# Kernel optimization log

Hardware: AMD Instinct MI355X
Metric: run time of the kernel (lower is better)

The kernel has to match this reference:

```python
import jax, jax.numpy as jnp
import numpy as np

N_NODES = 50000
IN_C, HID, N_CLS = 128, 128, 16
N_EDGES = 800000


def gcn_conv(x, W, b, src, dst, deg_inv_sqrt, n_nodes):
    # PyG GCNConv: h = x @ W; out[dst] += norm * h[src]; out += b
    h = x @ W                                   # [N, out_c]
    norm = deg_inv_sqrt[src] * deg_inv_sqrt[dst]  # [E]
    msgs = h[src] * norm[:, None]               # gather + scale, [E, out_c]
    out = jax.ops.segment_sum(msgs, dst, num_segments=n_nodes)
    return out + b


def setup_inputs() -> dict:
    key = jax.random.key(0)
    k1, k2, k3, k4, k5 = jax.random.split(key, 5)
    x = jax.random.normal(k1, (N_NODES, IN_C), dtype=jnp.float32)
    edge_index = jax.random.randint(k2, (2, N_EDGES), 0, N_NODES, dtype=jnp.int64)
    # glorot-ish params (torch.manual_seed(1234) in source only affects init values)
    def lin(k, fan_in, fan_out):
        s = 1.0 / np.sqrt(fan_in)
        kw, kb = jax.random.split(k)
        W = jax.random.uniform(kw, (fan_in, fan_out), minval=-s, maxval=s, dtype=jnp.float32)
        b = jax.random.uniform(kb, (fan_out,), minval=-s, maxval=s, dtype=jnp.float32)
        return W, b
    W1, b1 = lin(k3, IN_C, HID)
    W2, b2 = lin(k4, HID, HID)
    Wh, bh = lin(k5, HID, N_CLS)
    return {"x": x, "edge_index": edge_index, "W1": W1, "b1": b1,
            "W2": W2, "b2": b2, "Wh": Wh, "bh": bh}


def reference(x, edge_index, W1, b1, W2, b2, Wh, bh):
    n = x.shape[0]
    # add self-loops (PyG GCNConv default add_self_loops=True)
    loops = jnp.arange(n, dtype=edge_index.dtype)
    src = jnp.concatenate([edge_index[0], loops])
    dst = jnp.concatenate([edge_index[1], loops])
    # symmetric normalization D^{-1/2} (A+I) D^{-1/2}; degree over dst with unit weights
    deg = jax.ops.segment_sum(jnp.ones(src.shape[0], dtype=x.dtype), dst, num_segments=n)
    dis = jnp.where(deg > 0, jax.lax.rsqrt(deg), 0.0)
    h = gcn_conv(x, W1, b1, src, dst, dis, n)
    h = jax.nn.relu(h)
    h = gcn_conv(h, W2, b2, src, dst, dis, n)
    h = jax.nn.relu(h)
    return h @ Wh + bh
```

## Files before the change

### kernel.cpp

```cpp
#include <hip/hip_runtime.h>

#define CH 128
#define NCLS 16
#define CHK 16
#define NCHUNK 8
#define ECAP 131072

typedef __attribute__((ext_vector_type(8))) short bf16x8;
typedef __attribute__((ext_vector_type(4))) float f32x4;

__device__ inline ushort f2bf(float f) {
    unsigned u = __float_as_uint(f);
    unsigned r = u + 0x7fffu + ((u >> 16) & 1u);
    return (ushort)(r >> 16);
}
__device__ inline float bf2f(ushort b) {
    return __uint_as_float(((unsigned)b) << 16);
}

__global__ __launch_bounds__(256) void prep_kernel(
    const float* __restrict__ W1, const float* __restrict__ W2,
    ushort* __restrict__ w1hi, ushort* __restrict__ w1lo,
    ushort* __restrict__ w2hi, ushort* __restrict__ w2lo,
    int* __restrict__ cnt, int* __restrict__ pcnt, int* __restrict__ galloc,
    float* __restrict__ bufA, int n, int nbz) {
    int b = blockIdx.x, tid = threadIdx.x;
    if (b < 128) {
        const float* W = (b < 64) ? W1 : W2;
        ushort* Whi = (b < 64) ? w1hi : w2hi;
        ushort* Wlo = (b < 64) ? w1lo : w2lo;
        int t = ((b & 63) << 8) + tid;
        int k = t >> 7, nn = t & 127;
        float v = W[t];
        ushort h = f2bf(v);
        Whi[nn * CH + k] = h;
        Wlo[nn * CH + k] = f2bf(v - bf2f(h));
    } else if (b < 128 + nbz) {
        int i = (b - 128) * 256 + tid;
        if (i < n) cnt[i] = 0;
    } else {
        if (tid < NCHUNK * CHK) {
            int c = tid >> 4, ch = tid & 15;
            bufA[((size_t)c * (n + 1) + n) * CHK + ch] = 0.0f;
        }
        if (tid < 8) pcnt[tid] = 0;
        if (tid == 8) *galloc = 0;
    }
}

__global__ __launch_bounds__(256) void bucketcount_kernel(
    const int* __restrict__ src, const int* __restrict__ dst,
    unsigned* __restrict__ ebuf, int* __restrict__ pcnt,
    int* __restrict__ cnt, int E, float p8n) {
    __shared__ int lpos[8];
    __shared__ int lbase[8];
    int tid = threadIdx.x;
    if (tid < 8) lpos[tid] = 0;
    __syncthreads();
    int i0 = (blockIdx.x * 256 + tid) * 4;
    int part[4]; int off[4]; unsigned pk[4]; int c = 0;
    if (i0 + 3 < E) {
        int4 s4 = *(const int4*)&src[i0];
        int4 d4 = *(const int4*)&dst[i0];
        int ss[4] = {s4.x, s4.y, s4.z, s4.w};
        int dd[4] = {d4.x, d4.y, d4.z, d4.w};
        c = 4;
#pragma unroll
        for (int k = 0; k < 4; k++) {
            part[k] = min(7, (int)((float)dd[k] * p8n));
            pk[k] = ((unsigned)dd[k] << 16) | (unsigned)ss[k];
            off[k] = atomicAdd(&lpos[part[k]], 1);
            atomicAdd(&cnt[dd[k]], 1);
        }
    } else {
        for (int k = 0; k < 4 && i0 + k < E; k++) {
            int s = src[i0 + k], d = dst[i0 + k];
            part[c] = min(7, (int)((float)d * p8n));
            pk[c] = ((unsigned)d << 16) | (unsigned)s;
            off[c] = atomicAdd(&lpos[part[c]], 1);
            atomicAdd(&cnt[d], 1);
            c++;
        }
    }
    __syncthreads();
    if (tid < 8) lbase[tid] = atomicAdd(&pcnt[tid], lpos[tid]);
    __syncthreads();
    for (int k = 0; k < c; k++) {
        int idx = lbase[part[k]] + off[k];
        if (idx < ECAP) ebuf[(size_t)part[k] * ECAP + idx] = pk[k];
    }
}

__global__ __launch_bounds__(256) void place_kernel(
    const int* __restrict__ cnt, int* __restrict__ rsp,
    int* __restrict__ cursor, int* __restrict__ galloc,
    ushort* __restrict__ esrc, int n) {
    __shared__ int lds[256];
    __shared__ int gbase;
    int t = threadIdx.x;
    int i = blockIdx.x * 256 + t;
    int c = (i < n) ? cnt[i] : 0;
    int sz = (i < n) ? ((c + 8) & ~7) : 0;
    lds[t] = sz;
    __syncthreads();
    for (int off = 1; off < 256; off <<= 1) {
        int x = (t >= off) ? lds[t - off] : 0;
        __syncthreads();
        lds[t] += x;
        __syncthreads();
    }
    int incl = lds[t];
    if (t == 255) gbase = atomicAdd(galloc, incl);
    __syncthreads();
    int base = gbase + incl - sz;
    if (i < n) {
        rsp[i] = base;
        cursor[i] = base + 1;
        esrc[base] = (ushort)i;
        for (int p = base + 1 + c; p < base + sz; p++) esrc[p] = (ushort)n;
    }
}

template <bool RELU_IN>
__device__ __forceinline__ void gemm_body(
    int bx, int by, const float* __restrict__ A,
    const ushort* __restrict__ Bthi, const ushort* __restrict__ Btlo,
    const int* __restrict__ cntp, float* __restrict__ C, int n_rows) {
    const int tid = threadIdx.x;
    const int bm0 = bx * 128;
    const int wv = tid >> 6;
    const int lane = tid & 63;
    const int col = lane & 15;
    const int quad = lane >> 4;
    const int rbase = bm0 + wv * 32 + col;
    const int ntBase = by * 4;

    f32x4 acc[2][4];
#pragma unroll
    for (int m = 0; m < 2; m++)
#pragma unroll
        for (int t = 0; t < 4; t++) acc[m][t] = (f32x4){0.f, 0.f, 0.f, 0.f};

#pragma unroll
    for (int k0 = 0; k0 < 4; k0++) {
        const int kb = k0 * 32 + quad * 8;
        bf16x8 ah[2], al[2];
#pragma unroll
        for (int m = 0; m < 2; m++) {
            int arow = rbase + m * 16;
            bool av = (arow < n_rows);
            const float* __restrict__ Ap = A + (size_t)arow * CH + kb;
            float4 f0 = av ? *(const float4*)Ap       : make_float4(0.f, 0.f, 0.f, 0.f);
            float4 f1 = av ? *(const float4*)(Ap + 4) : make_float4(0.f, 0.f, 0.f, 0.f);
            if (RELU_IN) {
                f0.x = fmaxf(f0.x, 0.f); f0.y = fmaxf(f0.y, 0.f);
                f0.z = fmaxf(f0.z, 0.f); f0.w = fmaxf(f0.w, 0.f);
                f1.x = fmaxf(f1.x, 0.f); f1.y = fmaxf(f1.y, 0.f);
                f1.z = fmaxf(f1.z, 0.f); f1.w = fmaxf(f1.w, 0.f);
            }
            float fa[8] = {f0.x, f0.y, f0.z, f0.w, f1.x, f1.y, f1.z, f1.w};
#pragma unroll
            for (int j = 0; j < 8; j++) {
                ushort h = f2bf(fa[j]);
                ah[m][j] = (short)h;
                al[m][j] = (short)f2bf(fa[j] - bf2f(h));
            }
        }
#pragma unroll
        for (int t = 0; t < 4; t++) {
            const int boff = ((ntBase + t) * 16 + col) * CH + kb;
            bf16x8 bh = *(const bf16x8*)&Bthi[boff];
            bf16x8 bl = *(const bf16x8*)&Btlo[boff];
#pragma unroll
            for (int m = 0; m < 2; m++) {
                acc[m][t] = __builtin_amdgcn_mfma_f32_16x16x32_bf16(ah[m], bh, acc[m][t], 0, 0, 0);
                acc[m][t] = __builtin_amdgcn_mfma_f32_16x16x32_bf16(ah[m], bl, acc[m][t], 0, 0, 0);
                acc[m][t] = __builtin_amdgcn_mfma_f32_16x16x32_bf16(al[m], bh, acc[m][t], 0, 0, 0);
            }
        }
    }

#pragma unroll
    for (int m = 0; m < 2; m++) {
#pragma unroll
        for (int reg = 0; reg < 4; reg++) {
            int gr = bm0 + wv * 32 + m * 16 + quad * 4 + reg;
            if (gr < n_rows) {
                float d = rsqrtf((float)cntp[gr] + 1.0f);
#pragma unroll
                for (int t = 0; t < 4; t++) {
                    int nt = ntBase + t;
                    __builtin_nontemporal_store(
                        acc[m][t][reg] * d,
                        &C[((size_t)nt * (n_rows + 1) + gr) * CHK + col]);
                }
            }
        }
    }
}

template <bool RELU_IN>
__global__ __launch_bounds__(256, 4) void gemmfill_kernel(
    const float* __restrict__ A, const ushort* __restrict__ Bthi,
    const ushort* __restrict__ Btlo, const int* __restrict__ cntp,
    float* __restrict__ C, int n_rows, int nbx, int gemmBlocks,
    const unsigned* __restrict__ ebuf, const int* __restrict__ pcnt,
    int* __restrict__ cursor, ushort* __restrict__ esrc) {
    int b = blockIdx.x;
    if (b < gemmBlocks) {
        gemm_body<RELU_IN>(b % nbx, b / nbx, A, Bthi, Btlo, cntp, C, n_rows);
    } else {
        int fb = b - gemmBlocks;
        int part = fb & 7;
        int m = min(pcnt[part], ECAP);
        const unsigned* bk = ebuf + (size_t)part * ECAP;
        for (int e = (fb >> 3) * 256 + (int)threadIdx.x; e < m; e += 256 * 256) {
            unsigned pe = bk[e];
            int p = atomicAdd(&cursor[pe >> 16], 1);
            esrc[p] = (ushort)(pe & 0xffffu);
        }
    }
}

__global__ __launch_bounds__(256) void gather_kernel(
    const int* __restrict__ rsp, const int* __restrict__ cnt,
    const ushort* __restrict__ esrc, const float* __restrict__ hC,
    const float* __restrict__ bias, float* __restrict__ out, int n) {
    int c = blockIdx.x & 7;
    int wv = threadIdx.x >> 6;
    int lane = threadIdx.x & 63;
    int g = lane >> 2;
    int q = lane & 3;
    int i = (blockIdx.x >> 3) * 64 + wv * 16 + g;
    bool valid = (i < n);
    int iw = valid ? i : 0;
    const float4* __restrict__ h4 = (const float4*)(hC + (size_t)c * (n + 1) * CHK);

    float warm = 0.f;
    {
        int nblk = (n + 63) >> 6;
        size_t p = (size_t)(blockIdx.x >> 3) * 256 + threadIdx.x;
        size_t sliceF4 = ((size_t)(n + 1) * CHK) >> 2;
        for (; p < sliceF4; p += (size_t)nblk * 256) {
            float4 v = h4[p];
            warm += v.x + v.y + v.z + v.w;
        }
    }

    int beg = valid ? rsp[iw] : 0;
    int cv  = valid ? cnt[iw] : -8;
    int pc  = (cv + 8) & ~7;
    float4 acc = make_float4(0.f, 0.f, 0.f, 0.f);
    for (int j = beg; j < beg + pc; j += 8) {
        ushort4 e0 = *(const ushort4*)&esrc[j];
        ushort4 e1 = *(const ushort4*)&esrc[j + 4];
        float4 v0 = h4[(size_t)e0.x * 4 + q];
        float4 v1 = h4[(size_t)e0.y * 4 + q];
        float4 v2 = h4[(size_t)e0.z * 4 + q];
        float4 v3 = h4[(size_t)e0.w * 4 + q];
        float4 v4 = h4[(size_t)e1.x * 4 + q];
        float4 v5 = h4[(size_t)e1.y * 4 + q];
        float4 v6 = h4[(size_t)e1.z * 4 + q];
        float4 v7 = h4[(size_t)e1.w * 4 + q];
        acc.x += v0.x; acc.y += v0.y; acc.z += v0.z; acc.w += v0.w;
        acc.x += v1.x; acc.y += v1.y; acc.z += v1.z; acc.w += v1.w;
        acc.x += v2.x; acc.y += v2.y; acc.z += v2.z; acc.w += v2.w;
        acc.x += v3.x; acc.y += v3.y; acc.z += v3.z; acc.w += v3.w;
        acc.x += v4.x; acc.y += v4.y; acc.z += v4.z; acc.w += v4.w;
        acc.x += v5.x; acc.y += v5.y; acc.z += v5.z; acc.w += v5.w;
        acc.x += v6.x; acc.y += v6.y; acc.z += v6.z; acc.w += v6.w;
        acc.x += v7.x; acc.y += v7.y; acc.z += v7.z; acc.w += v7.w;
    }
    __asm__ volatile("" : : "v"(warm));
    if (valid) {
        float di = rsqrtf((float)cv + 1.0f);
        float4 bv = ((const float4*)bias)[c * 4 + q];
        f32x4 o;
        o[0] = bv.x + di * acc.x;
        o[1] = bv.y + di * acc.y;
        o[2] = bv.z + di * acc.z;
        o[3] = bv.w + di * acc.w;
        __builtin_nontemporal_store(o, (f32x4*)&((float4*)out)[(size_t)iw * 32 + c * 4 + q]);
    }
}

__global__ __launch_bounds__(256) void head_kernel(
    const float* __restrict__ A, const float* __restrict__ Wh,
    const float* __restrict__ bh, float* __restrict__ out, int n) {
    __shared__ float Ws[CH * NCLS];
    __shared__ float As[16][129];
    const int tid = threadIdx.x;
    const int n0 = blockIdx.x * 16;
#pragma unroll
    for (int i = 0; i < 8; i++) {
        int l = tid + i * 256;
        Ws[l] = Wh[l];
    }
#pragma unroll
    for (int i = 0; i < 8; i++) {
        int l = tid + i * 256;
        int r = l >> 7, c = l & 127;
        int gr = n0 + r;
        As[r][c] = (gr < n) ? fmaxf(A[(size_t)gr * CH + c], 0.0f) : 0.0f;
    }
    __syncthreads();
    int r = tid >> 4, c = tid & 15;
    float acc = bh[c];
#pragma unroll
    for (int k = 0; k < CH; k++) acc = fmaf(As[r][k], Ws[k * NCLS + c], acc);
    int gr = n0 + r;
    if (gr < n) out[(size_t)gr * NCLS + c] = acc;
}

extern "C" void kernel_launch(void* const* d_in, const int* in_sizes, int n_in,
                              void* d_out, int out_size, void* d_ws, size_t ws_size,
                              hipStream_t stream) {
    const float* x  = (const float*)d_in[0];
    const int*   ei = (const int*)d_in[1];
    const float* W1 = (const float*)d_in[2];
    const float* b1 = (const float*)d_in[3];
    const float* W2 = (const float*)d_in[4];
    const float* b2 = (const float*)d_in[5];
    const float* Wh = (const float*)d_in[6];
    const float* bh = (const float*)d_in[7];
    float* out = (float*)d_out;

    const int n = in_sizes[0] / CH;
    const int E = in_sizes[1] / 2;
    const int* src = ei;
    const int* dst = ei + E;

    ushort* w1hi = (ushort*)d_ws;
    ushort* w1lo = w1hi + CH * CH;
    ushort* w2hi = w1lo + CH * CH;
    ushort* w2lo = w2hi + CH * CH;
    float* bufA = (float*)(w2lo + CH * CH);
    float* bufB = bufA + (size_t)(n + 1) * CH;
    int* cnt    = (int*)(bufB + (size_t)n * CH);
    int* rsp    = cnt + n;
    int* cursor = rsp + n;
    int* pcnt   = cursor + n;
    int* galloc = pcnt + 8;
    ushort* esrc = (ushort*)(pcnt + 16);
    unsigned* ebuf = (unsigned*)bufB;

    const int B = 256;
    const int nbz = (n + B - 1) / B;
    const int nbx = (n + 127) / 128;
    const int gemmBlocks = nbx * 2;
    const float p8n = 8.0f / (float)n;

    prep_kernel<<<128 + nbz + 1, B, 0, stream>>>(W1, W2, w1hi, w1lo, w2hi, w2lo,
                                                 cnt, pcnt, galloc, bufA, n, nbz);
    bucketcount_kernel<<<(E + 1023) / 1024, B, 0, stream>>>(src, dst, ebuf, pcnt,
                                                            cnt, E, p8n);
    place_kernel<<<nbz, B, 0, stream>>>(cnt, rsp, cursor, galloc, esrc, n);

    const int gatherGrid = NCHUNK * ((n + 63) / 64);

    gemmfill_kernel<false><<<gemmBlocks + 2048, B, 0, stream>>>(
        x, w1hi, w1lo, cnt, bufA, n, nbx, gemmBlocks, ebuf, pcnt, cursor, esrc);
    gather_kernel<<<gatherGrid, B, 0, stream>>>(rsp, cnt, esrc, bufA, b1, bufB, n);
    gemmfill_kernel<true><<<gemmBlocks, B, 0, stream>>>(
        bufB, w2hi, w2lo, cnt, bufA, n, nbx, gemmBlocks, ebuf, pcnt, cursor, esrc);
    gather_kernel<<<gatherGrid, B, 0, stream>>>(rsp, cnt, esrc, bufA, b2, bufB, n);
    head_kernel<<<(n + 15) / 16, B, 0, stream>>>(bufB, Wh, bh, out, n);
}
```

Measured before the change: 296.4 us.

## Store intermediate GEMM output as fp16 and gather in 32-channel chunks

The GEMM epilogue now writes the degree-scaled hidden features as packed fp16 instead of fp32. The chunked layout changes from 8 chunks of 16 channels to 4 chunks of 32, so each gather lane loads 8 halves per neighbor and accumulates in fp32. This halves the bytes moved by the gather and the cache warm-up pass and halves the gather grid. In exchange it adds fp16 rounding error on the intermediate activations, and the output values could exceed fp16 range.

```diff
diff --git a/kernel.cpp b/kernel.cpp
--- a/kernel.cpp
+++ b/kernel.cpp
@@ -2,12 +2,13 @@
 
 #define CH 128
 #define NCLS 16
-#define CHK 16
-#define NCHUNK 8
+#define CHK 32
+#define NCHUNK 4
 #define ECAP 131072
 
 typedef __attribute__((ext_vector_type(8))) short bf16x8;
 typedef __attribute__((ext_vector_type(4))) float f32x4;
+typedef __attribute__((ext_vector_type(8))) _Float16 f16x8;
 
 __device__ inline ushort f2bf(float f) {
     unsigned u = __float_as_uint(f);
@@ -16,6 +17,12 @@
 }
 __device__ inline float bf2f(ushort b) {
     return __uint_as_float(((unsigned)b) << 16);
+}
+__device__ inline ushort f2h(float f) {
+    _Float16 h = (_Float16)f;
+    ushort u;
+    __builtin_memcpy(&u, &h, 2);
+    return u;
 }
 
 __global__ __launch_bounds__(256) void prep_kernel(
@@ -23,7 +30,7 @@
     ushort* __restrict__ w1hi, ushort* __restrict__ w1lo,
     ushort* __restrict__ w2hi, ushort* __restrict__ w2lo,
     int* __restrict__ cnt, int* __restrict__ pcnt, int* __restrict__ galloc,
-    float* __restrict__ bufA, int n, int nbz) {
+    ushort* __restrict__ hC, int n, int nbz) {
     int b = blockIdx.x, tid = threadIdx.x;
     if (b < 128) {
         const float* W = (b < 64) ? W1 : W2;
@@ -40,8 +47,8 @@
         if (i < n) cnt[i] = 0;
     } else {
         if (tid < NCHUNK * CHK) {
-            int c = tid >> 4, ch = tid & 15;
-            bufA[((size_t)c * (n + 1) + n) * CHK + ch] = 0.0f;
+            int c = tid >> 5, ch = tid & 31;
+            hC[((size_t)c * (n + 1) + n) * CHK + ch] = 0;
         }
         if (tid < 8) pcnt[tid] = 0;
         if (tid == 8) *galloc = 0;
@@ -125,7 +132,7 @@
 __device__ __forceinline__ void gemm_body(
     int bx, int by, const float* __restrict__ A,
     const ushort* __restrict__ Bthi, const ushort* __restrict__ Btlo,
-    const int* __restrict__ cntp, float* __restrict__ C, int n_rows) {
+    const int* __restrict__ cntp, ushort* __restrict__ C16, int n_rows) {
     const int tid = threadIdx.x;
     const int bm0 = bx * 128;
     const int wv = tid >> 6;
@@ -188,11 +195,15 @@
             if (gr < n_rows) {
                 float d = rsqrtf((float)cntp[gr] + 1.0f);
 #pragma unroll
-                for (int t = 0; t < 4; t++) {
-                    int nt = ntBase + t;
-                    __builtin_nontemporal_store(
-                        acc[m][t][reg] * d,
-                        &C[((size_t)nt * (n_rows + 1) + gr) * CHK + col]);
+                for (int tp = 0; tp < 4; tp += 2) {
+                    int nt0 = ntBase + tp;
+                    int chunk = nt0 >> 1;
+                    unsigned h0 = f2h(acc[m][tp][reg] * d);
+                    unsigned h1 = f2h(acc[m][tp + 1][reg] * d);
+                    unsigned pk = h0 | (h1 << 16);
+                    __builtin_nontemporal_store(pk,
+                        (unsigned*)&C16[((size_t)chunk * (n_rows + 1) + gr) * CHK
+                                        + 2 * col]);
                 }
             }
         }
@@ -203,12 +214,12 @@
 __global__ __launch_bounds__(256, 4) void gemmfill_kernel(
     const float* __restrict__ A, const ushort* __restrict__ Bthi,
     const ushort* __restrict__ Btlo, const int* __restrict__ cntp,
-    float* __restrict__ C, int n_rows, int nbx, int gemmBlocks,
+    ushort* __restrict__ C16, int n_rows, int nbx, int gemmBlocks,
     const unsigned* __restrict__ ebuf, const int* __restrict__ pcnt,
     int* __restrict__ cursor, ushort* __restrict__ esrc) {
     int b = blockIdx.x;
     if (b < gemmBlocks) {
-        gemm_body<RELU_IN>(b % nbx, b / nbx, A, Bthi, Btlo, cntp, C, n_rows);
+        gemm_body<RELU_IN>(b % nbx, b / nbx, A, Bthi, Btlo, cntp, C16, n_rows);
     } else {
         int fb = b - gemmBlocks;
         int part = fb & 7;
@@ -224,25 +235,27 @@
 
 __global__ __launch_bounds__(256) void gather_kernel(
     const int* __restrict__ rsp, const int* __restrict__ cnt,
-    const ushort* __restrict__ esrc, const float* __restrict__ hC,
+    const ushort* __restrict__ esrc, const ushort* __restrict__ hC16,
     const float* __restrict__ bias, float* __restrict__ out, int n) {
-    int c = blockIdx.x & 7;
+    int c = blockIdx.x & 3;
+    int bic = blockIdx.x >> 2;
     int wv = threadIdx.x >> 6;
     int lane = threadIdx.x & 63;
     int g = lane >> 2;
     int q = lane & 3;
-    int i = (blockIdx.x >> 3) * 64 + wv * 16 + g;
+    int i = bic * 64 + wv * 16 + g;
     bool valid = (i < n);
     int iw = valid ? i : 0;
-    const float4* __restrict__ h4 = (const float4*)(hC + (size_t)c * (n + 1) * CHK);
+    const f16x8* __restrict__ h8 = (const f16x8*)(hC16 + (size_t)c * (n + 1) * CHK);
 
     float warm = 0.f;
     {
-        int nblk = (n + 63) >> 6;
-        size_t p = (size_t)(blockIdx.x >> 3) * 256 + threadIdx.x;
-        size_t sliceF4 = ((size_t)(n + 1) * CHK) >> 2;
-        for (; p < sliceF4; p += (size_t)nblk * 256) {
-            float4 v = h4[p];
+        int nbr = (n + 63) >> 6;
+        const float4* __restrict__ w4 = (const float4*)h8;
+        size_t p = (size_t)bic * 256 + threadIdx.x;
+        size_t sliceF4 = ((size_t)(n + 1) * CHK) >> 3;
+        for (; p < sliceF4; p += (size_t)nbr * 256) {
+            float4 v = w4[p];
             warm += v.x + v.y + v.z + v.w;
         }
     }
@@ -250,37 +263,45 @@
     int beg = valid ? rsp[iw] : 0;
     int cv  = valid ? cnt[iw] : -8;
     int pc  = (cv + 8) & ~7;
-    float4 acc = make_float4(0.f, 0.f, 0.f, 0.f);
+    float accA[4] = {0.f, 0.f, 0.f, 0.f};
+    float accB[4] = {0.f, 0.f, 0.f, 0.f};
     for (int j = beg; j < beg + pc; j += 8) {
         ushort4 e0 = *(const ushort4*)&esrc[j];
         ushort4 e1 = *(const ushort4*)&esrc[j + 4];
-        float4 v0 = h4[(size_t)e0.x * 4 + q];
-        float4 v1 = h4[(size_t)e0.y * 4 + q];
-        float4 v2 = h4[(size_t)e0.z * 4 + q];
-        float4 v3 = h4[(size_t)e0.w * 4 + q];
-        float4 v4 = h4[(size_t)e1.x * 4 + q];
-        float4 v5 = h4[(size_t)e1.y * 4 + q];
-        float4 v6 = h4[(size_t)e1.z * 4 + q];
-        float4 v7 = h4[(size_t)e1.w * 4 + q];
-        acc.x += v0.x; acc.y += v0.y; acc.z += v0.z; acc.w += v0.w;
-        acc.x += v1.x; acc.y += v1.y; acc.z += v1.z; acc.w += v1.w;
-        acc.x += v2.x; acc.y += v2.y; acc.z += v2.z; acc.w += v2.w;
-        acc.x += v3.x; acc.y += v3.y; acc.z += v3.z; acc.w += v3.w;
-        acc.x += v4.x; acc.y += v4.y; acc.z += v4.z; acc.w += v4.w;
-        acc.x += v5.x; acc.y += v5.y; acc.z += v5.z; acc.w += v5.w;
-        acc.x += v6.x; acc.y += v6.y; acc.z += v6.z; acc.w += v6.w;
-        acc.x += v7.x; acc.y += v7.y; acc.z += v7.z; acc.w += v7.w;
+        f16x8 v0 = h8[(size_t)e0.x * 4 + q];
+        f16x8 v1 = h8[(size_t)e0.y * 4 + q];
+        f16x8 v2 = h8[(size_t)e0.z * 4 + q];
+        f16x8 v3 = h8[(size_t)e0.w * 4 + q];
+        f16x8 v4 = h8[(size_t)e1.x * 4 + q];
+        f16x8 v5 = h8[(size_t)e1.y * 4 + q];
+        f16x8 v6 = h8[(size_t)e1.z * 4 + q];
+        f16x8 v7 = h8[(size_t)e1.w * 4 + q];
+#pragma unroll
+        for (int s = 0; s < 4; s++) {
+            accA[s] += (float)v0[2 * s]; accB[s] += (float)v0[2 * s + 1];
+            accA[s] += (float)v1[2 * s]; accB[s] += (float)v1[2 * s + 1];
+            accA[s] += (float)v2[2 * s]; accB[s] += (float)v2[2 * s + 1];
+            accA[s] += (float)v3[2 * s]; accB[s] += (float)v3[2 * s + 1];
+            accA[s] += (float)v4[2 * s]; accB[s] += (float)v4[2 * s + 1];
+            accA[s] += (float)v5[2 * s]; accB[s] += (float)v5[2 * s + 1];
+            accA[s] += (float)v6[2 * s]; accB[s] += (float)v6[2 * s + 1];
+            accA[s] += (float)v7[2 * s]; accB[s] += (float)v7[2 * s + 1];
+        }
     }
     __asm__ volatile("" : : "v"(warm));
     if (valid) {
         float di = rsqrtf((float)cv + 1.0f);
-        float4 bv = ((const float4*)bias)[c * 4 + q];
-        f32x4 o;
-        o[0] = bv.x + di * acc.x;
-        o[1] = bv.y + di * acc.y;
-        o[2] = bv.z + di * acc.z;
-        o[3] = bv.w + di * acc.w;
-        __builtin_nontemporal_store(o, (f32x4*)&((float4*)out)[(size_t)iw * 32 + c * 4 + q]);
+        const float4* bias4 = (const float4*)bias;
+        float4 bvA = bias4[8 * c + q];
+        float4 bvB = bias4[8 * c + 4 + q];
+        f32x4 oA, oB;
+        oA[0] = bvA.x + di * accA[0]; oA[1] = bvA.y + di * accA[1];
+        oA[2] = bvA.z + di * accA[2]; oA[3] = bvA.w + di * accA[3];
+        oB[0] = bvB.x + di * accB[0]; oB[1] = bvB.y + di * accB[1];
+        oB[2] = bvB.z + di * accB[2]; oB[3] = bvB.w + di * accB[3];
+        float4* out4 = (float4*)out;
+        __builtin_nontemporal_store(oA, (f32x4*)&out4[(size_t)iw * 32 + 8 * c + q]);
+        __builtin_nontemporal_store(oB, (f32x4*)&out4[(size_t)iw * 32 + 8 * c + 4 + q]);
     }
 }
 
@@ -334,8 +355,8 @@
     ushort* w1lo = w1hi + CH * CH;
     ushort* w2hi = w1lo + CH * CH;
     ushort* w2lo = w2hi + CH * CH;
-    float* bufA = (float*)(w2lo + CH * CH);
-    float* bufB = bufA + (size_t)(n + 1) * CH;
+    ushort* hA  = w2lo + CH * CH;
+    float* bufB = (float*)(hA + (size_t)(n + 1) * CH);
     int* cnt    = (int*)(bufB + (size_t)n * CH);
     int* rsp    = cnt + n;
     int* cursor = rsp + n;
@@ -348,21 +369,21 @@
     const int nbz = (n + B - 1) / B;
     const int nbx = (n + 127) / 128;
     const int gemmBlocks = nbx * 2;
+    const int nbr = (n + 63) / 64;
+    const int gatherGrid = NCHUNK * nbr;
     const float p8n = 8.0f / (float)n;
 
     prep_kernel<<<128 + nbz + 1, B, 0, stream>>>(W1, W2, w1hi, w1lo, w2hi, w2lo,
-                                                 cnt, pcnt, galloc, bufA, n, nbz);
+                                                 cnt, pcnt, galloc, hA, n, nbz);
     bucketcount_kernel<<<(E + 1023) / 1024, B, 0, stream>>>(src, dst, ebuf, pcnt,
                                                             cnt, E, p8n);
     place_kernel<<<nbz, B, 0, stream>>>(cnt, rsp, cursor, galloc, esrc, n);
 
-    const int gatherGrid = NCHUNK * ((n + 63) / 64);
-
     gemmfill_kernel<false><<<gemmBlocks + 2048, B, 0, stream>>>(
-        x, w1hi, w1lo, cnt, bufA, n, nbx, gemmBlocks, ebuf, pcnt, cursor, esrc);
-    gather_kernel<<<gatherGrid, B, 0, stream>>>(rsp, cnt, esrc, bufA, b1, bufB, n);
+        x, w1hi, w1lo, cnt, hA, n, nbx, gemmBlocks, ebuf, pcnt, cursor, esrc);
+    gather_kernel<<<gatherGrid, B, 0, stream>>>(rsp, cnt, esrc, hA, b1, bufB, n);
     gemmfill_kernel<true><<<gemmBlocks, B, 0, stream>>>(
-        bufB, w2hi, w2lo, cnt, bufA, n, nbx, gemmBlocks, ebuf, pcnt, cursor, esrc);
-    gather_kernel<<<gatherGrid, B, 0, stream>>>(rsp, cnt, esrc, bufA, b2, bufB, n);
+        bufB, w2hi, w2lo, cnt, hA, n, nbx, gemmBlocks, ebuf, pcnt, cursor, esrc);
+    gather_kernel<<<gatherGrid, B, 0, stream>>>(rsp, cnt, esrc, hA, b2, bufB, n);
     head_kernel<<<(n + 15) / 16, B, 0, stream>>>(bufB, Wh, bh, out, n);
 }
```

New measurement: 262.6 us. 11.4% less time.
